# Kernel tuning notes

Measured on AMD Instinct MI355X. Metric: run time of the kernel, lower is better.

## Reference

```python
import jax, jax.numpy as jnp
import numpy as np

B, N, F, E, C, FC = 16, 5000, 512, 160000, 64, 128


def gcn_conv(x, src, dst, W, b, n_total):
    loop = jnp.arange(n_total, dtype=src.dtype)
    s = jnp.concatenate([src, loop])
    d = jnp.concatenate([dst, loop])
    deg = jax.ops.segment_sum(jnp.ones_like(s, dtype=x.dtype), d, num_segments=n_total)
    dinv = jnp.where(deg > 0, jax.lax.rsqrt(deg), 0.0)
    norm = dinv[s] * dinv[d]                      # [E']
    h = x @ W                                      # [n_total, out]
    msg = h[s] * norm[:, None]
    out = jax.ops.segment_sum(msg, d, num_segments=n_total)
    return out + b


def setup_inputs() -> dict:
    key = jax.random.key(0)
    ks = jax.random.split(key, 12)
    inp = {
        "node_features": jax.random.normal(ks[0], (B, N, F), jnp.float32),
        "col_features": jax.random.normal(ks[1], (B, C, FC), jnp.float32),
        "edge_index": jax.random.randint(ks[2], (2, E), 0, N, dtype=jnp.int64),
        # GCNConv 1/2 weights + node head
        "W1": jax.random.normal(ks[3], (F, 16), jnp.float32) / np.sqrt(F),
        "b1": jnp.zeros((16,), jnp.float32),
        "W2": jax.random.normal(ks[4], (16, 16), jnp.float32) / 4.0,
        "b2": jnp.zeros((16,), jnp.float32),
        "fc_w": jax.random.normal(ks[5], (16, 1), jnp.float32) / 4.0,
        "fc_b": jnp.zeros((1,), jnp.float32),
        # column MLP: Linear(FC,16) -> ReLU -> Linear(16,1)
        "cw1": jax.random.normal(ks[6], (FC, 16), jnp.float32) / np.sqrt(FC),
        "cb1": jnp.zeros((16,), jnp.float32),
        "cw2": jax.random.normal(ks[7], (16, 1), jnp.float32) / 4.0,
        "cb2": jnp.zeros((1,), jnp.float32),
    }
    return inp


def reference(node_features, col_features, edge_index, W1, b1, W2, b2, fc_w, fc_b, cw1, cb1, cw2, cb2):
    b, n, _ = node_features.shape
    n_total = b * n
    # batched edge_index via node-offset trick (shared graph per batch element)
    offsets = (jnp.arange(b, dtype=edge_index.dtype) * n)[:, None]   # [B,1]
    src = (edge_index[0][None, :] + offsets).reshape(-1)              # [B*E]
    dst = (edge_index[1][None, :] + offsets).reshape(-1)

    x = node_features.reshape(n_total, -1)
    x = jax.nn.relu(gcn_conv(x, src, dst, W1, b1, n_total))
    x = jax.nn.relu(gcn_conv(x, src, dst, W2, b2, n_total))
    node_logits = (x.reshape(b, n, 16) @ fc_w + fc_b)[..., 0]         # [B,N]

    h = jax.nn.relu(col_features @ cw1 + cb1)
    col_logits = (h @ cw2 + cb2)[..., 0]                              # [B,C]

    joint = node_logits[:, :, None] + col_logits[:, None, :]          # [B,N,C]
    return joint.reshape(b, -1)                                       # [B, N*C]
```

## Files before the change

kernel.cpp:

```cpp
#include <hip/hip_runtime.h>
#include <hip/hip_bf16.h>

typedef unsigned short u16;
typedef unsigned int   u32;
typedef __attribute__((ext_vector_type(8))) short bf16x8;
typedef __attribute__((ext_vector_type(4))) float f32x4;

#define B_  16
#define N_  5000
#define F_  512
#define C_  64
#define FC_ 128
#define NT  (B_ * N_)

__device__ __forceinline__ float bf2f(u16 h) {
    return __uint_as_float(((u32)h) << 16);
}
__device__ __forceinline__ u16 f2bf(float f) {
    union { __hip_bfloat16 h; u16 s; } c; c.h = __float2bfloat16(f); return c.s;
}
__device__ __forceinline__ float ldw(const void* p, int i, int fF) {
    return fF ? bf2f(((const u16*)p)[i]) : ((const float*)p)[i];
}

__global__ __launch_bounds__(256) void det_k(const u32* __restrict__ x32,
                                             const u32* __restrict__ ei32,
                                             int* __restrict__ flags)
{
    __shared__ int cnt;
    __shared__ int orv;
    if (threadIdx.x == 0) { cnt = 0; orv = 0; }
    __syncthreads();
    u32 w = x32[threadIdx.x];
    int e = (int)((w >> 7) & 0xffu);
    if (e >= 112 && e <= 136) atomicAdd(&cnt, 1);
    if (threadIdx.x < 32) {
        if (ei32[2 * threadIdx.x + 1] != 0u) atomicOr(&orv, 1);
    }
    __syncthreads();
    if (threadIdx.x == 0) {
        flags[0] = (cnt >= 128) ? 1 : 0;
        flags[1] = (orv == 0) ? 1 : 0;
    }
}

__device__ __forceinline__ int src_at(const u32* ei32, int t, int E, int fI) {
    return (int)(fI ? ei32[2 * t] : ei32[t]);
}
__device__ __forceinline__ int dst_at(const u32* ei32, int t, int E, int fI) {
    return (int)(fI ? ei32[2 * (E + t)] : ei32[E + t]);
}

__global__ __launch_bounds__(256) void prep_weights(
    const void* __restrict__ W1, const void* __restrict__ W2,
    const void* __restrict__ fcw, const void* __restrict__ cw1,
    const void* __restrict__ cw2, const void* __restrict__ b1,
    const void* __restrict__ b2, const void* __restrict__ fcb,
    const void* __restrict__ cb1, const void* __restrict__ cb2,
    const int* __restrict__ flags,
    float* __restrict__ w1f, float* __restrict__ w2f, float* __restrict__ fcwf,
    float* __restrict__ cw1f, float* __restrict__ cw2f, float* __restrict__ b1f,
    float* __restrict__ b2f, float* __restrict__ fcbf, float* __restrict__ cb1f,
    float* __restrict__ cb2f, u16* __restrict__ w1b)
{
    int fF = flags[0];
    int t = blockIdx.x * blockDim.x + threadIdx.x;
    if (t < 8192) { w1f[t] = ldw(W1, t, fF); return; }
    int u = t - 8192;
    if (u < 256)  { w2f[u]  = ldw(W2, u, fF);  return; }  u -= 256;
    if (u < 16)   { fcwf[u] = ldw(fcw, u, fF); return; }  u -= 16;
    if (u < 2048) { cw1f[u] = ldw(cw1, u, fF); return; }  u -= 2048;
    if (u < 16)   { cw2f[u] = ldw(cw2, u, fF); return; }  u -= 16;
    if (u < 16)   { b1f[u]  = ldw(b1, u, fF);  return; }  u -= 16;
    if (u < 16)   { b2f[u]  = ldw(b2, u, fF);  return; }  u -= 16;
    if (u < 1)    { fcbf[u] = ldw(fcb, u, fF); return; }  u -= 1;
    if (u < 16)   { cb1f[u] = ldw(cb1, u, fF); return; }  u -= 16;
    if (u < 1)    { cb2f[u] = ldw(cb2, u, fF); return; }  u -= 1;
    if (u < 8192) {
        int kb = u >> 9;
        int r  = (u >> 3) & 63;
        int j  = u & 7;
        w1b[u] = f2bf(ldw(W1, (kb * 32 + (r >> 4) * 8 + j) * 16 + (r & 15), fF));
    }
}

__global__ __launch_bounds__(256) void deg_k(const u32* __restrict__ ei32,
                                             const int* __restrict__ flags,
                                             int* __restrict__ deg, int E)
{
    int t = blockIdx.x * blockDim.x + threadIdx.x;
    if (t >= E) return;
    int d = dst_at(ei32, t, E, flags[1]);
    if ((unsigned)d < (unsigned)N_) atomicAdd(&deg[d], 1);
}

__global__ __launch_bounds__(1024) void scan_k(const int* __restrict__ deg,
                                               int* __restrict__ rowptr,
                                               int* __restrict__ cursor,
                                               float* __restrict__ dinv)
{
    __shared__ int ssum[1024];
    int t = threadIdx.x;
    int base = t * 5;
    int loc[5];
    int run = 0;
#pragma unroll
    for (int i = 0; i < 5; i++) {
        int idx = base + i;
        int v = (idx < N_) ? deg[idx] : 0;
        loc[i] = run;
        run += v;
    }
    ssum[t] = run;
    __syncthreads();
    for (int offs = 1; offs < 1024; offs <<= 1) {
        int v = (t >= offs) ? ssum[t - offs] : 0;
        __syncthreads();
        ssum[t] += v;
        __syncthreads();
    }
    int exclusive = ssum[t] - run;
#pragma unroll
    for (int i = 0; i < 5; i++) {
        int idx = base + i;
        if (idx < N_) {
            int rp = exclusive + loc[i];
            rowptr[idx] = rp;
            cursor[idx] = rp;
            dinv[idx] = 1.0f / sqrtf((float)deg[idx] + 1.0f);
        }
    }
    if (t == 1023) rowptr[N_] = ssum[1023];
}

__global__ __launch_bounds__(256) void fill_k(const u32* __restrict__ ei32,
                                              const int* __restrict__ flags,
                                              int* __restrict__ cursor,
                                              int* __restrict__ csr, int E)
{
    int t = blockIdx.x * blockDim.x + threadIdx.x;
    if (t >= E) return;
    int fI = flags[1];
    int s = src_at(ei32, t, E, fI);
    int d = dst_at(ei32, t, E, fI);
    if ((unsigned)d >= (unsigned)N_) return;
    if ((unsigned)s >= (unsigned)N_) s = 0;
    int pos = atomicAdd(&cursor[d], 1);
    if ((unsigned)pos < (unsigned)E) csr[pos] = s;
}

__global__ __launch_bounds__(256, 6) void gemm1_k(const void* __restrict__ xraw,
                                                  const float* __restrict__ w1f,
                                                  const u16* __restrict__ w1b,
                                                  const float* __restrict__ dinv,
                                                  const int* __restrict__ flags,
                                                  u16* __restrict__ out)
{
    __shared__ float smem[4352];
    const int t    = threadIdx.x;
    const int lane = t & 63;
    const int wv   = t >> 6;
    const int row0 = blockIdx.x * 64;
    const int fF   = flags[0];

    if (fF) {
        const u16* xb = (const u16*)xraw;
        bf16x8 bfr[16];
#pragma unroll
        for (int kb = 0; kb < 16; kb++)
            bfr[kb] = *(const bf16x8*)(w1b + kb * 512 + lane * 8);

        f32x4 acc = {0.0f, 0.0f, 0.0f, 0.0f};
        const u16* xr = xb + (size_t)(row0 + wv * 16 + (lane & 15)) * F_
                           + (lane >> 4) * 8;
#pragma unroll
        for (int kb = 0; kb < 16; kb++) {
            bf16x8 a = *(const bf16x8*)(xr + kb * 32);
            acc = __builtin_amdgcn_mfma_f32_16x16x32_bf16(a, bfr[kb], acc, 0, 0, 0);
        }
#pragma unroll
        for (int i = 0; i < 4; i++) {
            int grow = row0 + wv * 16 + (lane >> 4) * 4 + i;
            int n  = grow % N_;
            int bb = grow / N_;
            out[(size_t)n * 256 + bb * 16 + (lane & 15)] = f2bf(acc[i] * dinv[n]);
        }
        return;
    }

    float acc[16];
#pragma unroll
    for (int k = 0; k < 16; k++) acc[k] = 0.0f;

    const int wvu = __builtin_amdgcn_readfirstlane(wv);

    for (int c = 0; c < 8; c++) {
        __syncthreads();
        const float* xf = (const float*)xraw + c * 64;
#pragma unroll
        for (int i = 0; i < 4; i++) {
            int u = i * 256 + t;
            int r = u >> 4, c4 = u & 15;
            float4 v = *(const float4*)(xf + (size_t)(row0 + r) * F_ + c4 * 4);
            float* dp = &smem[r * 65 + c4 * 4];
            dp[0] = v.x; dp[1] = v.y; dp[2] = v.z; dp[3] = v.w;
        }
        __syncthreads();
        const float* xr = &smem[lane * 65 + wvu * 16];
        const float* wr = w1f + (c * 64 + wvu * 16) * 16;
#pragma unroll
        for (int f = 0; f < 16; f++) {
            float xv = xr[f];
#pragma unroll
            for (int k = 0; k < 16; k++) acc[k] += xv * wr[f * 16 + k];
        }
    }

    __syncthreads();
    float (*red)[64][17] = (float (*)[64][17])smem;
#pragma unroll
    for (int k = 0; k < 16; k++) red[wv][lane][k] = acc[k];
    __syncthreads();

    int r  = t >> 2;
    int kc = (t & 3) * 4;
    int row = row0 + r;
    int n = row % N_;
    int b = row / N_;
    float s = dinv[n];
    union { uint2 u; u16 h[4]; } o;
#pragma unroll
    for (int k = 0; k < 4; k++) {
        float v = red[0][r][kc + k] + red[1][r][kc + k]
                + red[2][r][kc + k] + red[3][r][kc + k];
        o.h[k] = f2bf(v * s);
    }
    *(uint2*)(out + (size_t)n * 256 + b * 16 + kc) = o.u;
}

__global__ __launch_bounds__(256) void agg1_k(const u16* __restrict__ h,
                                              const int* __restrict__ rowptr,
                                              const int* __restrict__ csr,
                                              const float* __restrict__ dinv,
                                              const float* __restrict__ b1f,
                                              const float* __restrict__ w2f,
                                              u16* __restrict__ out)
{
    int d   = blockIdx.x;
    int tid = threadIdx.x;
    int k   = tid & 15;
    float acc = bf2f(h[(size_t)d * 256 + tid]);
    int e0 = rowptr[d], e1 = rowptr[d + 1];
    for (int base = e0; base < e1; base += 8) {
        int idx[8];
#pragma unroll
        for (int j = 0; j < 8; j++) {
            int e = base + j;
            idx[j] = csr[e < e1 ? e : e0];
        }
        float v[8];
#pragma unroll
        for (int j = 0; j < 8; j++) v[j] = bf2f(h[(size_t)idx[j] * 256 + tid]);
#pragma unroll
        for (int j = 0; j < 8; j++) if (base + j < e1) acc += v[j];
    }
    float dv = dinv[d];
    float x1 = fmaxf(acc * dv + b1f[k], 0.0f);
    float h2 = 0.0f;
#pragma unroll
    for (int j = 0; j < 16; j++) {
        float xj = __shfl(x1, j, 16);
        h2 += xj * w2f[j * 16 + k];
    }
    out[(size_t)d * 256 + tid] = f2bf(h2 * dv);
}

__global__ __launch_bounds__(256) void agg2_k(const u16* __restrict__ h,
                                              const int* __restrict__ rowptr,
                                              const int* __restrict__ csr,
                                              const float* __restrict__ dinv,
                                              const float* __restrict__ b2f,
                                              const float* __restrict__ fcwf,
                                              const float* __restrict__ fcbf,
                                              float* __restrict__ nl)
{
    int d   = blockIdx.x;
    int tid = threadIdx.x;
    int k   = tid & 15;
    int b   = tid >> 4;
    float acc = bf2f(h[(size_t)d * 256 + tid]);
    int e0 = rowptr[d], e1 = rowptr[d + 1];
    for (int base = e0; base < e1; base += 8) {
        int idx[8];
#pragma unroll
        for (int j = 0; j < 8; j++) {
            int e = base + j;
            idx[j] = csr[e < e1 ? e : e0];
        }
        float v[8];
#pragma unroll
        for (int j = 0; j < 8; j++) v[j] = bf2f(h[(size_t)idx[j] * 256 + tid]);
#pragma unroll
        for (int j = 0; j < 8; j++) if (base + j < e1) acc += v[j];
    }
    float x2 = fmaxf(acc * dinv[d] + b2f[k], 0.0f);
    float p = x2 * fcwf[k];
    p += __shfl_xor(p, 8, 16);
    p += __shfl_xor(p, 4, 16);
    p += __shfl_xor(p, 2, 16);
    p += __shfl_xor(p, 1, 16);
    if (k == 0) nl[b * N_ + d] = p + fcbf[0];
}

__global__ __launch_bounds__(256) void col_k(const void* __restrict__ cfraw,
                                             const float* __restrict__ cw1f,
                                             const float* __restrict__ cb1f,
                                             const float* __restrict__ cw2f,
                                             const float* __restrict__ cb2f,
                                             const int* __restrict__ flags,
                                             float* __restrict__ cl)
{
    int t = blockIdx.x * blockDim.x + threadIdx.x;
    if (t >= B_ * C_) return;
    float acc[16];
#pragma unroll
    for (int k = 0; k < 16; k++) acc[k] = cb1f[k];
    if (flags[0]) {
        const u16* r = (const u16*)cfraw + (size_t)t * FC_;
        for (int f = 0; f < FC_; f += 8) {
            uint4 pk = *(const uint4*)(r + f);
            u32 q[4] = {pk.x, pk.y, pk.z, pk.w};
#pragma unroll
            for (int j = 0; j < 4; j++) {
                float v0 = bf2f((u16)(q[j] & 0xffffu));
                float v1 = bf2f((u16)(q[j] >> 16));
                const float* w0 = cw1f + (f + 2 * j) * 16;
#pragma unroll
                for (int k = 0; k < 16; k++) acc[k] += v0 * w0[k];
#pragma unroll
                for (int k = 0; k < 16; k++) acc[k] += v1 * w0[16 + k];
            }
        }
    } else {
        const float* r = (const float*)cfraw + (size_t)t * FC_;
        for (int f = 0; f < FC_; f += 4) {
            float4 a = *(const float4*)(r + f);
            float v[4] = {a.x, a.y, a.z, a.w};
#pragma unroll
            for (int j = 0; j < 4; j++) {
                const float* w0 = cw1f + (f + j) * 16;
#pragma unroll
                for (int k = 0; k < 16; k++) acc[k] += v[j] * w0[k];
            }
        }
    }
    float s = cb2f[0];
#pragma unroll
    for (int k = 0; k < 16; k++) s += fmaxf(acc[k], 0.0f) * cw2f[k];
    cl[t] = s;
}

__global__ __launch_bounds__(256) void join_k(const float* __restrict__ nl,
                                              const float* __restrict__ cl,
                                              const int* __restrict__ flags,
                                              void* __restrict__ outraw)
{
    int t = blockIdx.x * blockDim.x + threadIdx.x;
    if (t >= NT * C_ / 8) return;
    int g  = t >> 3;
    int c0 = (t & 7) * 8;
    int b  = g / N_;
    float nv = nl[g];
    const float* c = cl + b * C_ + c0;
    float4 a0 = *(const float4*)c;
    float4 a1 = *(const float4*)(c + 4);
    float v[8] = {a0.x, a0.y, a0.z, a0.w, a1.x, a1.y, a1.z, a1.w};
#pragma unroll
    for (int i = 0; i < 8; i++) v[i] += nv;
    size_t idx = (size_t)g * C_ + c0;
    if (flags[0]) {
        union { uint4 u; u16 h[8]; } pkv;
#pragma unroll
        for (int i = 0; i < 8; i++) pkv.h[i] = f2bf(v[i]);
        *(uint4*)((u16*)outraw + idx) = pkv.u;
    } else {
        float* o = (float*)outraw + idx;
        *(float4*)o       = make_float4(v[0], v[1], v[2], v[3]);
        *(float4*)(o + 4) = make_float4(v[4], v[5], v[6], v[7]);
    }
}

extern "C" void kernel_launch(void* const* d_in, const int* in_sizes, int n_in,
                              void* d_out, int out_size, void* d_ws, size_t ws_size,
                              hipStream_t stream)
{
    const void* x    = d_in[0];
    const void* cf   = d_in[1];
    const u32*  ei32 = (const u32*)d_in[2];
    const void* W1   = d_in[3];
    const void* b1   = d_in[4];
    const void* W2   = d_in[5];
    const void* b2   = d_in[6];
    const void* fcw  = d_in[7];
    const void* fcb  = d_in[8];
    const void* cw1  = d_in[9];
    const void* cb1  = d_in[10];
    const void* cw2  = d_in[11];
    const void* cb2  = d_in[12];

    const int E = in_sizes[2] / 2;

    char* base = (char*)d_ws;
    size_t off = 0;
    auto alloc = [&](size_t bytes) -> void* {
        void* p = base + off;
        off = (off + bytes + 255) & ~(size_t)255;
        return p;
    };
    int*   flags  = (int*)alloc(2 * 4);
    float* w1f  = (float*)alloc(8192 * 4);
    u16*   w1b  = (u16*)alloc(8192 * 2);
    float* w2f  = (float*)alloc(256 * 4);
    float* fcwf = (float*)alloc(16 * 4);
    float* cw1f = (float*)alloc(2048 * 4);
    float* cw2f = (float*)alloc(16 * 4);
    float* b1f  = (float*)alloc(16 * 4);
    float* b2f  = (float*)alloc(16 * 4);
    float* fcbf = (float*)alloc(4);
    float* cb1f = (float*)alloc(16 * 4);
    float* cb2f = (float*)alloc(4);
    int*   deg    = (int*)alloc((size_t)N_ * 4);
    int*   rowptr = (int*)alloc((size_t)(N_ + 1) * 4);
    int*   cursor = (int*)alloc((size_t)N_ * 4);
    float* dinv   = (float*)alloc((size_t)N_ * 4);
    int*   csr    = (int*)alloc((size_t)E * 4);
    u16*   bufA = (u16*)alloc((size_t)NT * 16 * 2);
    u16*   bufB = (u16*)alloc((size_t)NT * 16 * 2);
    float* nl   = (float*)alloc((size_t)NT * 4);
    float* cl   = (float*)alloc((size_t)B_ * C_ * 4);

    det_k<<<1, 256, 0, stream>>>((const u32*)x, ei32, flags);
    hipMemsetAsync(deg, 0, (size_t)N_ * 4, stream);
    prep_weights<<<(10578 + 8192 + 255) / 256, 256, 0, stream>>>(
        W1, W2, fcw, cw1, cw2, b1, b2, fcb, cb1, cb2, flags,
        w1f, w2f, fcwf, cw1f, cw2f, b1f, b2f, fcbf, cb1f, cb2f, w1b);
    deg_k<<<(E + 255) / 256, 256, 0, stream>>>(ei32, flags, deg, E);
    scan_k<<<1, 1024, 0, stream>>>(deg, rowptr, cursor, dinv);
    fill_k<<<(E + 255) / 256, 256, 0, stream>>>(ei32, flags, cursor, csr, E);

    gemm1_k<<<NT / 64, 256, 0, stream>>>(x, w1f, w1b, dinv, flags, bufA);
    agg1_k<<<N_, 256, 0, stream>>>(bufA, rowptr, csr, dinv, b1f, w2f, bufB);
    agg2_k<<<N_, 256, 0, stream>>>(bufB, rowptr, csr, dinv, b2f, fcwf, fcbf, nl);
    col_k<<<(B_ * C_ + 255) / 256, 256, 0, stream>>>(cf, cw1f, cb1f, cw2f, cb2f, flags, cl);
    join_k<<<(NT * C_ / 8 + 255) / 256, 256, 0, stream>>>(nl, cl, flags, d_out);
}
```

Before: 363.4 us.

## Split GEMM1 K dimension across two blocks with separate reduction kernel

Splits the 512-wide feature reduction of the first GCN projection into two halves, each computed by its own block, doubling the grid. Partial fp32 results go to a new scratch buffer, and a new kernel sums them, applies the degree normalization, converts to bf16 and writes the transposed layout. This aims to add parallelism and memory-level concurrency to the x-reading GEMM, which is bandwidth-bound on a ~160MB input. In exchange it adds an extra launch and about 10MB of extra partial-buffer traffic.

```diff
diff --git a/kernel.cpp b/kernel.cpp
--- a/kernel.cpp
+++ b/kernel.cpp
@@ -152,38 +152,38 @@
 __global__ __launch_bounds__(256, 6) void gemm1_k(const void* __restrict__ xraw,
                                                   const float* __restrict__ w1f,
                                                   const u16* __restrict__ w1b,
-                                                  const float* __restrict__ dinv,
                                                   const int* __restrict__ flags,
-                                                  u16* __restrict__ out)
+                                                  float* __restrict__ pbuf)
 {
     __shared__ float smem[4352];
     const int t    = threadIdx.x;
     const int lane = t & 63;
     const int wv   = t >> 6;
-    const int row0 = blockIdx.x * 64;
+    const int half = blockIdx.x & 1;
+    const int row0 = (blockIdx.x >> 1) * 64;
+    const int fbase = half * 256;
     const int fF   = flags[0];
+    float* pb = pbuf + (size_t)half * NT * 16;
 
     if (fF) {
         const u16* xb = (const u16*)xraw;
-        bf16x8 bfr[16];
-#pragma unroll
-        for (int kb = 0; kb < 16; kb++)
-            bfr[kb] = *(const bf16x8*)(w1b + kb * 512 + lane * 8);
+        bf16x8 bfr[8];
+#pragma unroll
+        for (int kb = 0; kb < 8; kb++)
+            bfr[kb] = *(const bf16x8*)(w1b + (half * 8 + kb) * 512 + lane * 8);
 
         f32x4 acc = {0.0f, 0.0f, 0.0f, 0.0f};
         const u16* xr = xb + (size_t)(row0 + wv * 16 + (lane & 15)) * F_
-                           + (lane >> 4) * 8;
-#pragma unroll
-        for (int kb = 0; kb < 16; kb++) {
+                           + fbase + (lane >> 4) * 8;
+#pragma unroll
+        for (int kb = 0; kb < 8; kb++) {
             bf16x8 a = *(const bf16x8*)(xr + kb * 32);
             acc = __builtin_amdgcn_mfma_f32_16x16x32_bf16(a, bfr[kb], acc, 0, 0, 0);
         }
 #pragma unroll
         for (int i = 0; i < 4; i++) {
             int grow = row0 + wv * 16 + (lane >> 4) * 4 + i;
-            int n  = grow % N_;
-            int bb = grow / N_;
-            out[(size_t)n * 256 + bb * 16 + (lane & 15)] = f2bf(acc[i] * dinv[n]);
+            pb[(size_t)grow * 16 + (lane & 15)] = acc[i];
         }
         return;
     }
@@ -194,9 +194,9 @@
 
     const int wvu = __builtin_amdgcn_readfirstlane(wv);
 
-    for (int c = 0; c < 8; c++) {
+    for (int c = 0; c < 4; c++) {
         __syncthreads();
-        const float* xf = (const float*)xraw + c * 64;
+        const float* xf = (const float*)xraw + fbase + c * 64;
 #pragma unroll
         for (int i = 0; i < 4; i++) {
             int u = i * 256 + t;
@@ -207,7 +207,7 @@
         }
         __syncthreads();
         const float* xr = &smem[lane * 65 + wvu * 16];
-        const float* wr = w1f + (c * 64 + wvu * 16) * 16;
+        const float* wr = w1f + (fbase + c * 64 + wvu * 16) * 16;
 #pragma unroll
         for (int f = 0; f < 16; f++) {
             float xv = xr[f];
@@ -224,18 +224,34 @@
 
     int r  = t >> 2;
     int kc = (t & 3) * 4;
-    int row = row0 + r;
-    int n = row % N_;
-    int b = row / N_;
+    float4 o;
+    o.x = red[0][r][kc+0] + red[1][r][kc+0] + red[2][r][kc+0] + red[3][r][kc+0];
+    o.y = red[0][r][kc+1] + red[1][r][kc+1] + red[2][r][kc+1] + red[3][r][kc+1];
+    o.z = red[0][r][kc+2] + red[1][r][kc+2] + red[2][r][kc+2] + red[3][r][kc+2];
+    o.w = red[0][r][kc+3] + red[1][r][kc+3] + red[2][r][kc+3] + red[3][r][kc+3];
+    *(float4*)(pb + (size_t)(row0 + r) * 16 + kc) = o;
+}
+
+__global__ __launch_bounds__(256) void greduce_k(const float* __restrict__ pbuf,
+                                                 const float* __restrict__ dinv,
+                                                 u16* __restrict__ out)
+{
+    int t = blockIdx.x * blockDim.x + threadIdx.x;
+    if (t >= NT * 4) return;
+    int i = t * 4;
+    int row = i >> 4;
+    int kc  = i & 15;
+    float4 a = *(const float4*)(pbuf + i);
+    float4 b = *(const float4*)(pbuf + (size_t)NT * 16 + i);
+    int n  = row % N_;
+    int bb = row / N_;
     float s = dinv[n];
     union { uint2 u; u16 h[4]; } o;
-#pragma unroll
-    for (int k = 0; k < 4; k++) {
-        float v = red[0][r][kc + k] + red[1][r][kc + k]
-                + red[2][r][kc + k] + red[3][r][kc + k];
-        o.h[k] = f2bf(v * s);
-    }
-    *(uint2*)(out + (size_t)n * 256 + b * 16 + kc) = o.u;
+    o.h[0] = f2bf((a.x + b.x) * s);
+    o.h[1] = f2bf((a.y + b.y) * s);
+    o.h[2] = f2bf((a.z + b.z) * s);
+    o.h[3] = f2bf((a.w + b.w) * s);
+    *(uint2*)(out + (size_t)n * 256 + bb * 16 + kc) = o.u;
 }
 
 __global__ __launch_bounds__(256) void agg1_k(const u16* __restrict__ h,
@@ -434,6 +450,7 @@
     int*   cursor = (int*)alloc((size_t)N_ * 4);
     float* dinv   = (float*)alloc((size_t)N_ * 4);
     int*   csr    = (int*)alloc((size_t)E * 4);
+    float* pbuf = (float*)alloc((size_t)2 * NT * 16 * 4);
     u16*   bufA = (u16*)alloc((size_t)NT * 16 * 2);
     u16*   bufB = (u16*)alloc((size_t)NT * 16 * 2);
     float* nl   = (float*)alloc((size_t)NT * 4);
@@ -448,7 +465,8 @@
     scan_k<<<1, 1024, 0, stream>>>(deg, rowptr, cursor, dinv);
     fill_k<<<(E + 255) / 256, 256, 0, stream>>>(ei32, flags, cursor, csr, E);
 
-    gemm1_k<<<NT / 64, 256, 0, stream>>>(x, w1f, w1b, dinv, flags, bufA);
+    gemm1_k<<<2 * (NT / 64), 256, 0, stream>>>(x, w1f, w1b, flags, pbuf);
+    greduce_k<<<(NT * 4 + 255) / 256, 256, 0, stream>>>(pbuf, dinv, bufA);
     agg1_k<<<N_, 256, 0, stream>>>(bufA, rowptr, csr, dinv, b1f, w2f, bufB);
     agg2_k<<<N_, 256, 0, stream>>>(bufB, rowptr, csr, dinv, b2f, fcwf, fcbf, nl);
     col_k<<<(B_ * C_ + 255) / 256, 256, 0, stream>>>(cf, cw1f, cb1f, cw2f, cb2f, flags, cl);
```

Result: no change. 366.5 us (+0.8%).
